# Optimization experiments

Measured on AMD Instinct MI355X. Metric: run time of the kernel, lower is better.

The kernel has to match this reference:

```python
import jax, jax.numpy as jnp
import numpy as np

EMBED = 256
HEADS = 8
HDIM = 32
FF = 1024
EPS = 1e-6
EVERY = 8        # stock_attn_every
LAST_DENSE = 16  # stock_attn_last_dense
B, N, T = 2, 256, 256


def rmsnorm(x, w):
    return x * jax.lax.rsqrt(jnp.mean(x * x, axis=-1, keepdims=True) + EPS) * w


def mha(x, Wq, Wk, Wv, Wo, mask=None):
    # x: (B, S, D); mask: (B, S) bool key-padding mask (True = keep)
    b, s, _ = x.shape
    q = (x @ Wq).reshape(b, s, HEADS, HDIM)
    k = (x @ Wk).reshape(b, s, HEADS, HDIM)
    v = (x @ Wv).reshape(b, s, HEADS, HDIM)
    scores = jnp.einsum('bqhd,bkhd->bhqk', q, k) * (HDIM ** -0.5)
    if mask is not None:
        scores = jnp.where(mask[:, None, None, :], scores, jnp.asarray(-1e9, scores.dtype))
    attn = jax.nn.softmax(scores, axis=-1)
    out = jnp.einsum('bhqk,bkhd->bqhd', attn, v).reshape(b, s, HEADS * HDIM)
    return out @ Wo


def active_t(t):
    # static index set: sparse strided steps + last dense window
    lds = max(0, t - LAST_DENSE)
    idx = sorted(set(list(range(0, lds, max(1, EVERY))) + list(range(lds, t))))
    return jnp.asarray(idx, dtype=jnp.int32)


def setup_inputs() -> dict:
    key = jax.random.key(0)
    ks = jax.random.split(key, 16)
    p = lambda k, shape: (jax.random.normal(k, shape, dtype=jnp.float32) * 0.02)
    inp = {
        'h': jax.random.normal(ks[0], (B, N, T, EMBED), dtype=jnp.float32),
        'stock_mask': jnp.ones((B, N), dtype=jnp.int32),
        'norm_t_w': jnp.ones((EMBED,), dtype=jnp.float32),
        'norm_s_w': jnp.ones((EMBED,), dtype=jnp.float32),
        'norm_ff_w': jnp.ones((EMBED,), dtype=jnp.float32),
        'Wq_t': p(ks[1], (EMBED, HEADS * HDIM)),
        'Wk_t': p(ks[2], (EMBED, HEADS * HDIM)),
        'Wv_t': p(ks[3], (EMBED, HEADS * HDIM)),
        'Wo_t': p(ks[4], (HEADS * HDIM, EMBED)),
        'Wq_s': p(ks[5], (EMBED, HEADS * HDIM)),
        'Wk_s': p(ks[6], (EMBED, HEADS * HDIM)),
        'Wv_s': p(ks[7], (EMBED, HEADS * HDIM)),
        'Wo_s': p(ks[8], (HEADS * HDIM, EMBED)),
        'W1': p(ks[9], (EMBED, FF)),
        'b1': jnp.zeros((FF,), dtype=jnp.float32),
        'W2': p(ks[10], (FF, EMBED)),
        'b2': jnp.zeros((EMBED,), dtype=jnp.float32),
    }
    return inp


def reference(h, stock_mask, norm_t_w, norm_s_w, norm_ff_w,
              Wq_t, Wk_t, Wv_t, Wo_t, Wq_s, Wk_s, Wv_s, Wo_s,
              W1, b1, W2, b2):
    b, n, t, d = h.shape
    # --- time attention (per stock, dense over T) ---
    h_t = rmsnorm(h.reshape(b * n, t, d), norm_t_w)
    h = h + mha(h_t, Wq_t, Wk_t, Wv_t, Wo_t).reshape(b, n, t, d)
    # --- sparse-T gather -> stock attention -> scatter back ---
    active = active_t(t)
    tp = active.shape[0]
    h_s = h[:, :, active, :].transpose(0, 2, 1, 3).reshape(b * tp, n, d)
    m = jnp.broadcast_to(stock_mask.astype(bool)[:, None, :], (b, tp, n)).reshape(b * tp, n)
    h_s = mha(rmsnorm(h_s, norm_s_w), Wq_s, Wk_s, Wv_s, Wo_s, mask=m)
    h = h.at[:, :, active, :].add(h_s.reshape(b, tp, n, d).transpose(0, 2, 1, 3))
    # --- FFN ---
    x = rmsnorm(h, norm_ff_w)
    return h + (jax.nn.gelu(x @ W1 + b1) @ W2 + b2)
```

## Files before the change

### kernel.cpp

```cpp
#include <hip/hip_runtime.h>
#include <hip/hip_bf16.h>

typedef __attribute__((ext_vector_type(8))) short short8;
typedef __attribute__((ext_vector_type(4))) float f32x4;

#define TP 46

__device__ __forceinline__ unsigned short f2bf(float f) {
  unsigned int u = __float_as_uint(f);
  u = (u + 0x7fff + ((u >> 16) & 1)) >> 16;
  return (unsigned short)u;
}
__device__ __forceinline__ unsigned short f2bf_fast(float f) {
  return (unsigned short)((__float_as_uint(f) + 0x8000u) >> 16);
}
__device__ __forceinline__ float bf2f(short u) {
  return __uint_as_float((unsigned)(unsigned short)u << 16);
}
__device__ __forceinline__ float fast_rcp(float x) {
#if __has_builtin(__builtin_amdgcn_rcpf)
  return __builtin_amdgcn_rcpf(x);
#else
  return 1.0f / x;
#endif
}
__device__ __forceinline__ float fast_rsq(float x) {
#if __has_builtin(__builtin_amdgcn_rsqf)
  return __builtin_amdgcn_rsqf(x);
#else
  return rsqrtf(x);
#endif
}

__device__ __forceinline__ int act_t(int j) { return j < 30 ? (j << 3) : (210 + j); }

__device__ __forceinline__ void load_lds16(const unsigned short* g, unsigned short* lds_base) {
#if __has_builtin(__builtin_amdgcn_global_load_lds)
  __builtin_amdgcn_global_load_lds(
      (const __attribute__((address_space(1))) unsigned int*)(unsigned long long)g,
      (__attribute__((address_space(3))) unsigned int*)(unsigned int)(unsigned long long)lds_base,
      16, 0, 0);
#else
  int lane = threadIdx.x & 63;
  *(short8*)(lds_base + lane * 8) = *(const short8*)g;
#endif
}

__global__ __launch_bounds__(256) void convw_kernel(
    const float* __restrict__ wq_t, const float* __restrict__ wk_t,
    const float* __restrict__ wv_t, const float* __restrict__ wo_t,
    const float* __restrict__ wq_s, const float* __restrict__ wk_s,
    const float* __restrict__ wv_s, const float* __restrict__ wo_s,
    const float* __restrict__ w1, const float* __restrict__ w2,
    unsigned short* __restrict__ pool) {
  int idx = blockIdx.x * 256 + threadIdx.x;
  float v;
  if (idx < 524288) {
    int tile = idx >> 12, local = idx & 4095;
    int ks = local >> 9, q = local & 511;
    int l = q >> 3, e = q & 7;
    int lr = l & 15, lg = l >> 4;
    int ct = tile & 15, grp = tile >> 4;
    const float* s = (grp == 0) ? wq_t : (grp == 1) ? wk_t : (grp == 2) ? wv_t :
                     (grp == 3) ? wo_t : (grp == 4) ? wq_s : (grp == 5) ? wk_s :
                     (grp == 6) ? wv_s : wo_s;
    v = s[(size_t)(ks * 32 + lg * 8 + e) * 256 + ct * 16 + lr];
  } else if (idx < 786432) {
    int local = idx - 524288;
    int e = local & 7, t = local >> 3;
    int lane = t & 63, ks = (t >> 6) & 7, ct = (t >> 9) & 1, fc = t >> 10;
    int lr = lane & 15, lg = lane >> 4;
    v = w1[(size_t)(ks * 32 + lg * 8 + e) * 1024 + fc * 32 + ct * 16 + lr];
  } else {
    int local = idx - 786432;
    int e2 = local & 7, t = local >> 3;
    int lane = t & 63, ct2 = (t >> 6) & 15, fc = t >> 10;
    int lr = lane & 15, lg = lane >> 4;
    v = w2[(size_t)(fc * 32 + lg * 8 + e2) * 256 + ct2 * 16 + lr];
  }
  pool[idx] = f2bf(v);
}

template<int GATHER>
__global__ __launch_bounds__(256) void qkv_kernel(
    const float* __restrict__ src, const float* __restrict__ nw,
    const unsigned short* __restrict__ WF,
    unsigned short* __restrict__ qb, unsigned short* __restrict__ kb,
    unsigned short* __restrict__ vb, int row_base) {
  __shared__ __align__(16) unsigned short Wbuf[2][4096];
  int tid = threadIdx.x, wv = tid >> 6, lane = tid & 63, lr = lane & 15, lg = lane >> 4;
  int row0 = blockIdx.x * 128 + wv * 32;
  short8 afrag[2][8];
  #pragma unroll
  for (int rt = 0; rt < 2; ++rt) {
    int lrow = row0 + rt * 16 + lr;
    const float* rp;
    if (GATHER) {
      int gr = row_base + lrow;
      int b = gr / 11776; int rem = gr - b * 11776;
      int j = rem >> 8, n = rem & 255;
      rp = src + (((size_t)((b << 8) + n) << 8) + act_t(j)) * 256;
    } else {
      rp = src + (size_t)lrow * 256;
    }
    float4 x[16];
    #pragma unroll
    for (int ks = 0; ks < 8; ++ks) {
      x[ks * 2]     = *(const float4*)(rp + ks * 32 + lg * 8);
      x[ks * 2 + 1] = *(const float4*)(rp + ks * 32 + lg * 8 + 4);
    }
    float ss = 0.f;
    #pragma unroll
    for (int i = 0; i < 16; ++i)
      ss += x[i].x * x[i].x + x[i].y * x[i].y + x[i].z * x[i].z + x[i].w * x[i].w;
    ss += __shfl_xor(ss, 16, 64);
    ss += __shfl_xor(ss, 32, 64);
    float sc = fast_rsq(ss * 0.00390625f + 1e-6f);
    #pragma unroll
    for (int ks = 0; ks < 8; ++ks) {
      float4 w0 = *(const float4*)(nw + ks * 32 + lg * 8);
      float4 w1_ = *(const float4*)(nw + ks * 32 + lg * 8 + 4);
      short8 af;
      af[0] = (short)f2bf_fast(x[ks * 2].x * sc * w0.x);
      af[1] = (short)f2bf_fast(x[ks * 2].y * sc * w0.y);
      af[2] = (short)f2bf_fast(x[ks * 2].z * sc * w0.z);
      af[3] = (short)f2bf_fast(x[ks * 2].w * sc * w0.w);
      af[4] = (short)f2bf_fast(x[ks * 2 + 1].x * sc * w1_.x);
      af[5] = (short)f2bf_fast(x[ks * 2 + 1].y * sc * w1_.y);
      af[6] = (short)f2bf_fast(x[ks * 2 + 1].z * sc * w1_.z);
      af[7] = (short)f2bf_fast(x[ks * 2 + 1].w * sc * w1_.w);
      afrag[rt][ks] = af;
    }
  }
  #pragma unroll
  for (int i = 0; i < 2; ++i) {
    int s = wv * 2 + i;
    load_lds16(WF + s * 512 + lane * 8, &Wbuf[0][s * 512]);
  }
  f32x4 zero = {0.f, 0.f, 0.f, 0.f};
  for (int t = 0; t < 48; ++t) {
    __syncthreads();
    if (t < 47) {
      #pragma unroll
      for (int i = 0; i < 2; ++i) {
        int s = wv * 2 + i;
        load_lds16(WF + (size_t)(t + 1) * 4096 + s * 512 + lane * 8,
                   &Wbuf[(t + 1) & 1][s * 512]);
      }
    }
    const unsigned short* Ws = &Wbuf[t & 1][0];
    f32x4 a0 = zero, a1 = zero;
    #pragma unroll
    for (int ks = 0; ks < 8; ++ks) {
      short8 bw = *(const short8*)&Ws[ks * 512 + lane * 8];
      a0 = __builtin_amdgcn_mfma_f32_16x16x32_bf16(bw, afrag[0][ks], a0, 0, 0, 0);
      a1 = __builtin_amdgcn_mfma_f32_16x16x32_bf16(bw, afrag[1][ks], a1, 0, 0, 0);
    }
    int m = t >> 4, ct = t & 15;
    unsigned short* dst = (m == 0) ? qb : (m == 1) ? kb : vb;
    ushort4 p0, p1;
    p0.x = f2bf_fast(a0[0]); p0.y = f2bf_fast(a0[1]);
    p0.z = f2bf_fast(a0[2]); p0.w = f2bf_fast(a0[3]);
    p1.x = f2bf_fast(a1[0]); p1.y = f2bf_fast(a1[1]);
    p1.z = f2bf_fast(a1[2]); p1.w = f2bf_fast(a1[3]);
    *(ushort4*)(dst + (size_t)(row0 + lr) * 256 + ct * 16 + lg * 4) = p0;
    *(ushort4*)(dst + (size_t)(row0 + 16 + lr) * 256 + ct * 16 + lg * 4) = p1;
  }
}

template<int MODE>
__global__ __launch_bounds__(256) void gemm256_kernel(
    const unsigned short* __restrict__ X, const unsigned short* __restrict__ WF,
    const float* __restrict__ resid, float* __restrict__ outf, int row_base) {
  __shared__ __align__(16) unsigned short Wbuf[2][4096];
  int tid = threadIdx.x, wv = tid >> 6, lane = tid & 63, lr = lane & 15, lg = lane >> 4;
  int row0 = blockIdx.x * 128 + wv * 32;
  short8 afrag[2][8];
  size_t rb[2];
  #pragma unroll
  for (int rt = 0; rt < 2; ++rt) {
    int row = row0 + rt * 16 + lr;
    #pragma unroll
    for (int ks = 0; ks < 8; ++ks)
      afrag[rt][ks] = *(const short8*)(X + (size_t)row * 256 + ks * 32 + lg * 8);
    if (MODE == 1) {
      rb[rt] = (size_t)row * 256;
    } else {
      int gr = row_base + row;
      int b = gr / 11776; int rem = gr - b * 11776;
      int j = rem >> 8, n = rem & 255;
      rb[rt] = (((size_t)((b << 8) + n) << 8) + act_t(j)) * 256;
    }
  }
  #pragma unroll
  for (int i = 0; i < 2; ++i) {
    int s = wv * 2 + i;
    load_lds16(WF + s * 512 + lane * 8, &Wbuf[0][s * 512]);
  }
  f32x4 zero = {0.f, 0.f, 0.f, 0.f};
  for (int t = 0; t < 16; ++t) {
    __syncthreads();
    if (t < 15) {
      #pragma unroll
      for (int i = 0; i < 2; ++i) {
        int s = wv * 2 + i;
        load_lds16(WF + (size_t)(t + 1) * 4096 + s * 512 + lane * 8,
                   &Wbuf[(t + 1) & 1][s * 512]);
      }
    }
    const unsigned short* Ws = &Wbuf[t & 1][0];
    f32x4 a0 = zero, a1 = zero;
    #pragma unroll
    for (int ks = 0; ks < 8; ++ks) {
      short8 bw = *(const short8*)&Ws[ks * 512 + lane * 8];
      a0 = __builtin_amdgcn_mfma_f32_16x16x32_bf16(bw, afrag[0][ks], a0, 0, 0, 0);
      a1 = __builtin_amdgcn_mfma_f32_16x16x32_bf16(bw, afrag[1][ks], a1, 0, 0, 0);
    }
    int col = t * 16 + lg * 4;
    if (MODE == 1) {
      float4 r0 = *(const float4*)(resid + rb[0] + col);
      float4 r1 = *(const float4*)(resid + rb[1] + col);
      float4 o0, o1;
      o0.x = r0.x + a0[0]; o0.y = r0.y + a0[1]; o0.z = r0.z + a0[2]; o0.w = r0.w + a0[3];
      o1.x = r1.x + a1[0]; o1.y = r1.y + a1[1]; o1.z = r1.z + a1[2]; o1.w = r1.w + a1[3];
      *(float4*)(outf + rb[0] + col) = o0;
      *(float4*)(outf + rb[1] + col) = o1;
    } else {
      float4 c0 = *(const float4*)(outf + rb[0] + col);
      float4 c1 = *(const float4*)(outf + rb[1] + col);
      c0.x += a0[0]; c0.y += a0[1]; c0.z += a0[2]; c0.w += a0[3];
      c1.x += a1[0]; c1.y += a1[1]; c1.z += a1[2]; c1.w += a1[3];
      *(float4*)(outf + rb[0] + col) = c0;
      *(float4*)(outf + rb[1] + col) = c1;
    }
  }
}

__global__ __launch_bounds__(256) void attn_kernel(
    const unsigned short* __restrict__ Q, const unsigned short* __restrict__ K,
    const unsigned short* __restrict__ V, unsigned short* __restrict__ O,
    const int* __restrict__ mask, int seq_base) {
  __shared__ unsigned short Ksh[256][40];
  __shared__ unsigned short Vtsh[32][264];
  __shared__ unsigned short Psh[4][16][264];
  int head = blockIdx.x, seq = blockIdx.y;
  int hc = head * 32;
  size_t sb = (size_t)seq * 65536;
  int tid = threadIdx.x;
  {
    int r = tid;
    #pragma unroll
    for (int c = 0; c < 4; ++c) {
      *(short8*)&Ksh[r][c * 8] = *(const short8*)(K + sb + (size_t)r * 256 + hc + c * 8);
      short8 vv = *(const short8*)(V + sb + (size_t)r * 256 + hc + c * 8);
      #pragma unroll
      for (int e = 0; e < 8; ++e) Vtsh[c * 8 + e][r] = (unsigned short)vv[e];
    }
  }
  __syncthreads();
  int wv = tid >> 6, lane = tid & 63, lr = lane & 15, lg = lane >> 4;
  const float scale = 0.17677669529663687f;
  int mb = 0;
  if (mask) mb = (seq_base + seq) / TP;
  f32x4 zero = {0.f, 0.f, 0.f, 0.f};
  for (int rt = 0; rt < 4; ++rt) {
    int row0 = wv * 64 + rt * 16;
    short8 aq = *(const short8*)(Q + sb + (size_t)(row0 + lr) * 256 + hc + lg * 8);
    f32x4 s[16];
    #pragma unroll
    for (int ct = 0; ct < 16; ++ct) {
      short8 kb = *(const short8*)&Ksh[ct * 16 + lr][lg * 8];
      s[ct] = __builtin_amdgcn_mfma_f32_16x16x32_bf16(kb, aq, zero, 0, 0, 0);
    }
    #pragma unroll
    for (int ct = 0; ct < 16; ++ct) {
      if (mask) {
        const int4 m4 = *(const int4*)(mask + mb * 256 + ct * 16 + lg * 4);
        s[ct][0] = m4.x ? s[ct][0] * scale : -1e9f;
        s[ct][1] = m4.y ? s[ct][1] * scale : -1e9f;
        s[ct][2] = m4.z ? s[ct][2] * scale : -1e9f;
        s[ct][3] = m4.w ? s[ct][3] * scale : -1e9f;
      } else {
        #pragma unroll
        for (int r = 0; r < 4; ++r) s[ct][r] *= scale;
      }
    }
    float mx = -3e38f;
    #pragma unroll
    for (int ct = 0; ct < 16; ++ct)
      #pragma unroll
      for (int r = 0; r < 4; ++r) mx = fmaxf(mx, s[ct][r]);
    mx = fmaxf(mx, __shfl_xor(mx, 16, 64));
    mx = fmaxf(mx, __shfl_xor(mx, 32, 64));
    float sum = 0.f;
    #pragma unroll
    for (int ct = 0; ct < 16; ++ct)
      #pragma unroll
      for (int r = 0; r < 4; ++r) {
        float p = __expf(s[ct][r] - mx);
        s[ct][r] = p; sum += p;
      }
    sum += __shfl_xor(sum, 16, 64);
    sum += __shfl_xor(sum, 32, 64);
    float inv = fast_rcp(sum);
    #pragma unroll
    for (int ct = 0; ct < 16; ++ct) {
      ushort4 pk;
      pk.x = f2bf_fast(s[ct][0] * inv); pk.y = f2bf_fast(s[ct][1] * inv);
      pk.z = f2bf_fast(s[ct][2] * inv); pk.w = f2bf_fast(s[ct][3] * inv);
      *(ushort4*)&Psh[wv][lr][ct * 16 + lg * 4] = pk;
    }
    f32x4 o[2] = {zero, zero};
    #pragma unroll
    for (int ks = 0; ks < 8; ++ks) {
      short8 pa = *(const short8*)&Psh[wv][lr][ks * 32 + lg * 8];
      #pragma unroll
      for (int c2 = 0; c2 < 2; ++c2) {
        short8 vbf = *(const short8*)&Vtsh[c2 * 16 + lr][ks * 32 + lg * 8];
        o[c2] = __builtin_amdgcn_mfma_f32_16x16x32_bf16(vbf, pa, o[c2], 0, 0, 0);
      }
    }
    #pragma unroll
    for (int c2 = 0; c2 < 2; ++c2) {
      ushort4 ok;
      ok.x = f2bf_fast(o[c2][0]); ok.y = f2bf_fast(o[c2][1]);
      ok.z = f2bf_fast(o[c2][2]); ok.w = f2bf_fast(o[c2][3]);
      *(ushort4*)(O + sb + (size_t)(row0 + lr) * 256 + hc + c2 * 16 + lg * 4) = ok;
    }
  }
}

__global__ __launch_bounds__(256, 4) void ffn_kernel(
    float* __restrict__ hio, const float* __restrict__ nw,
    const unsigned short* __restrict__ W1F, const unsigned short* __restrict__ W2F,
    const float* __restrict__ b1, const float* __restrict__ b2) {
  __shared__ __align__(16) unsigned short Wbuf[16384];
  __shared__ __align__(16) unsigned short Psh[4][16][36];
  int tid = threadIdx.x;
  int wv = tid >> 6, lane = tid & 63, lr = lane & 15, lg = lane >> 4;
  int wrow = blockIdx.x * 64 + wv * 16;
  const float* rp = hio + (size_t)(wrow + lr) * 256;
  short8 xfrag[8];
  float ss = 0.f;
  #pragma unroll
  for (int ks = 0; ks < 8; ++ks) {
    float4 a = *(const float4*)(rp + ks * 32 + lg * 8);
    float4 b = *(const float4*)(rp + ks * 32 + lg * 8 + 4);
    ss += a.x * a.x + a.y * a.y + a.z * a.z + a.w * a.w;
    ss += b.x * b.x + b.y * b.y + b.z * b.z + b.w * b.w;
    short8 xf;
    xf[0] = (short)f2bf_fast(a.x); xf[1] = (short)f2bf_fast(a.y);
    xf[2] = (short)f2bf_fast(a.z); xf[3] = (short)f2bf_fast(a.w);
    xf[4] = (short)f2bf_fast(b.x); xf[5] = (short)f2bf_fast(b.y);
    xf[6] = (short)f2bf_fast(b.z); xf[7] = (short)f2bf_fast(b.w);
    xfrag[ks] = xf;
  }
  ss += __shfl_xor(ss, 16, 64);
  ss += __shfl_xor(ss, 32, 64);
  float sc = fast_rsq(ss * 0.00390625f + 1e-6f);
  #pragma unroll
  for (int ks = 0; ks < 8; ++ks) {
    float4 wa = *(const float4*)(nw + ks * 32 + lg * 8);
    float4 wb = *(const float4*)(nw + ks * 32 + lg * 8 + 4);
    short8 xf = xfrag[ks], af;
    af[0] = (short)f2bf_fast(bf2f(xf[0]) * sc * wa.x);
    af[1] = (short)f2bf_fast(bf2f(xf[1]) * sc * wa.y);
    af[2] = (short)f2bf_fast(bf2f(xf[2]) * sc * wa.z);
    af[3] = (short)f2bf_fast(bf2f(xf[3]) * sc * wa.w);
    af[4] = (short)f2bf_fast(bf2f(xf[4]) * sc * wb.x);
    af[5] = (short)f2bf_fast(bf2f(xf[5]) * sc * wb.y);
    af[6] = (short)f2bf_fast(bf2f(xf[6]) * sc * wb.z);
    af[7] = (short)f2bf_fast(bf2f(xf[7]) * sc * wb.w);
    xfrag[ks] = af;
  }
  f32x4 zero = {0.f, 0.f, 0.f, 0.f};
  f32x4 oacc[16];
  #pragma unroll
  for (int ct = 0; ct < 16; ++ct) oacc[ct] = zero;
  for (int fc = 0; fc < 32; ++fc) {
    __syncthreads();
    #pragma unroll
    for (int i = 0; i < 8; ++i) {
      int s = wv * 8 + i;
      const unsigned short* srcp = (s < 16) ? (W1F + (size_t)fc * 8192 + s * 512)
                                            : (W2F + (size_t)fc * 8192 + (s - 16) * 512);
      load_lds16(srcp + lane * 8, &Wbuf[s * 512]);
    }
    __syncthreads();
    const unsigned short* W1s = &Wbuf[0];
    const unsigned short* W2s = &Wbuf[8192];
    f32x4 hacc[2];
    hacc[0] = zero; hacc[1] = zero;
    #pragma unroll
    for (int ks = 0; ks < 8; ++ks) {
      #pragma unroll
      for (int ct = 0; ct < 2; ++ct) {
        short8 w1f = *(const short8*)&W1s[(ct * 8 + ks) * 512 + lane * 8];
        hacc[ct] = __builtin_amdgcn_mfma_f32_16x16x32_bf16(w1f, xfrag[ks], hacc[ct], 0, 0, 0);
      }
    }
    #pragma unroll
    for (int ct = 0; ct < 2; ++ct) {
      float4 bb = *(const float4*)(b1 + fc * 32 + ct * 16 + lg * 4);
      ushort4 pk;
      float hv = hacc[ct][0] + bb.x;
      pk.x = f2bf_fast(hv * fast_rcp(1.0f + __expf(-1.5957691216057308f * fmaf(0.044715f * hv, hv * hv, hv))));
      hv = hacc[ct][1] + bb.y;
      pk.y = f2bf_fast(hv * fast_rcp(1.0f + __expf(-1.5957691216057308f * fmaf(0.044715f * hv, hv * hv, hv))));
      hv = hacc[ct][2] + bb.z;
      pk.z = f2bf_fast(hv * fast_rcp(1.0f + __expf(-1.5957691216057308f * fmaf(0.044715f * hv, hv * hv, hv))));
      hv = hacc[ct][3] + bb.w;
      pk.w = f2bf_fast(hv * fast_rcp(1.0f + __expf(-1.5957691216057308f * fmaf(0.044715f * hv, hv * hv, hv))));
      *(ushort4*)&Psh[wv][lr][ct * 16 + lg * 4] = pk;
    }
    short8 pa = *(const short8*)&Psh[wv][lr][lg * 8];
    #pragma unroll
    for (int ct2 = 0; ct2 < 16; ++ct2) {
      short8 bw2 = *(const short8*)&W2s[ct2 * 512 + lane * 8];
      oacc[ct2] = __builtin_amdgcn_mfma_f32_16x16x32_bf16(bw2, pa, oacc[ct2], 0, 0, 0);
    }
  }
  size_t rbase = (size_t)(wrow + lr) * 256;
  #pragma unroll
  for (int ct2 = 0; ct2 < 16; ++ct2) {
    int col = ct2 * 16 + lg * 4;
    float4 bb2 = *(const float4*)(b2 + col);
    float4 cur = *(const float4*)(hio + rbase + col);
    cur.x += oacc[ct2][0] + bb2.x;
    cur.y += oacc[ct2][1] + bb2.y;
    cur.z += oacc[ct2][2] + bb2.z;
    cur.w += oacc[ct2][3] + bb2.w;
    *(float4*)(hio + rbase + col) = cur;
  }
}

extern "C" void kernel_launch(void* const* d_in, const int* in_sizes, int n_in,
                              void* d_out, int out_size, void* d_ws, size_t ws_size,
                              hipStream_t stream) {
  (void)in_sizes; (void)n_in; (void)out_size;
  const float* h   = (const float*)d_in[0];
  const int* smask = (const int*)d_in[1];
  const float* ntw = (const float*)d_in[2];
  const float* nsw = (const float*)d_in[3];
  const float* nfw = (const float*)d_in[4];
  const float* wq_t = (const float*)d_in[5];
  const float* wk_t = (const float*)d_in[6];
  const float* wv_t = (const float*)d_in[7];
  const float* wo_t = (const float*)d_in[8];
  const float* wq_s = (const float*)d_in[9];
  const float* wk_s = (const float*)d_in[10];
  const float* wv_s = (const float*)d_in[11];
  const float* wo_s = (const float*)d_in[12];
  const float* w1  = (const float*)d_in[13];
  const float* b1  = (const float*)d_in[14];
  const float* w2  = (const float*)d_in[15];
  const float* b2  = (const float*)d_in[16];
  float* out = (float*)d_out;
  unsigned short* pool = (unsigned short*)d_ws;

  unsigned short* WQKVtF = pool;
  unsigned short* WOtF   = pool + 196608;
  unsigned short* WQKVsF = pool + 262144;
  unsigned short* WOsF   = pool + 458752;
  unsigned short* W1F    = pool + 524288;
  unsigned short* W2F    = pool + 786432;

  size_t wbytes = 1048576ull * 2;
  size_t avail = (ws_size > wbytes) ? (ws_size - wbytes) : 0;
  long long scl = (long long)(avail / 524288ull);
  int SC = scl < 1 ? 1 : (scl > 512 ? 512 : (int)scl);
  unsigned short* xnorm = pool + 1048576;
  unsigned short* qb = xnorm + (size_t)SC * 65536;
  unsigned short* kb = qb + (size_t)SC * 65536;
  unsigned short* vb = kb + (size_t)SC * 65536;

  convw_kernel<<<4096, 256, 0, stream>>>(wq_t, wk_t, wv_t, wo_t, wq_s, wk_s, wv_s,
                                         wo_s, w1, w2, pool);

  for (int s0 = 0; s0 < 512; s0 += SC) {
    int ns = (512 - s0 < SC) ? (512 - s0) : SC;
    int rows = ns * 256;
    qkv_kernel<0><<<rows / 128, 256, 0, stream>>>(h + (size_t)s0 * 65536, ntw, WQKVtF,
                                                  qb, kb, vb, 0);
    attn_kernel<<<dim3(8, ns), 256, 0, stream>>>(qb, kb, vb, xnorm, nullptr, 0);
    gemm256_kernel<1><<<rows / 128, 256, 0, stream>>>(xnorm, WOtF,
        h + (size_t)s0 * 65536, out + (size_t)s0 * 65536, 0);
  }

  int SC2 = SC < 92 ? SC : 92;
  for (int s0 = 0; s0 < 92; s0 += SC2) {
    int ns = (92 - s0 < SC2) ? (92 - s0) : SC2;
    int rows = ns * 256;
    qkv_kernel<1><<<rows / 128, 256, 0, stream>>>(out, nsw, WQKVsF, qb, kb, vb, s0 * 256);
    attn_kernel<<<dim3(8, ns), 256, 0, stream>>>(qb, kb, vb, xnorm, smask, s0);
    gemm256_kernel<2><<<rows / 128, 256, 0, stream>>>(xnorm, WOsF, nullptr, out, s0 * 256);
  }

  ffn_kernel<<<2048, 256, 0, stream>>>(out, nfw, W1F, W2F, b1, b2);
}
```

Before: 755.7 us.

## Double-buffer FFN weight tiles with manual vmcnt waits and template attention mask

The FFN kernel now double-buffers its W1/W2 LDS tiles, prefetching the next chunk while computing the current one. It uses raw s_barrier plus s_waitcnt vmcnt instead of full __syncthreads, and caches b1 in shared memory. The qkv kernel gets the same finer-grained waits, the attention kernel takes the mask as a template parameter and uses a coalesced K/V load pattern, and the FFN launch is split into two halves. The double buffer doubles FFN LDS use, which may lower occupancy, and the hand-written waitcnt counts must match the number of outstanding loads or results will be wrong.

Measured after the change: 835.8 us. 10.6% more time.

```diff
diff --git a/kernel.cpp b/kernel.cpp
--- a/kernel.cpp
+++ b/kernel.cpp
@@ -5,6 +5,11 @@
 typedef __attribute__((ext_vector_type(4))) float f32x4;
 
 #define TP 46
+
+#define SBAR() asm volatile("s_barrier" ::: "memory")
+#define VMCNT2() asm volatile("s_waitcnt vmcnt(2)" ::: "memory")
+#define VMCNT8() asm volatile("s_waitcnt vmcnt(8)" ::: "memory")
+#define VMCNT0() asm volatile("s_waitcnt vmcnt(0)" ::: "memory")
 
 __device__ __forceinline__ unsigned short f2bf(float f) {
   unsigned int u = __float_as_uint(f);
@@ -139,7 +144,7 @@
   }
   f32x4 zero = {0.f, 0.f, 0.f, 0.f};
   for (int t = 0; t < 48; ++t) {
-    __syncthreads();
+    SBAR();
     if (t < 47) {
       #pragma unroll
       for (int i = 0; i < 2; ++i) {
@@ -147,7 +152,11 @@
         load_lds16(WF + (size_t)(t + 1) * 4096 + s * 512 + lane * 8,
                    &Wbuf[(t + 1) & 1][s * 512]);
       }
-    }
+      VMCNT2();
+    } else {
+      VMCNT0();
+    }
+    SBAR();
     const unsigned short* Ws = &Wbuf[t & 1][0];
     f32x4 a0 = zero, a1 = zero;
     #pragma unroll
@@ -208,6 +217,7 @@
                    &Wbuf[(t + 1) & 1][s * 512]);
       }
     }
+    __syncthreads();
     const unsigned short* Ws = &Wbuf[t & 1][0];
     f32x4 a0 = zero, a1 = zero;
     #pragma unroll
@@ -236,6 +246,7 @@
   }
 }
 
+template<int MASKED>
 __global__ __launch_bounds__(256) void attn_kernel(
     const unsigned short* __restrict__ Q, const unsigned short* __restrict__ K,
     const unsigned short* __restrict__ V, unsigned short* __restrict__ O,
@@ -248,9 +259,10 @@
   size_t sb = (size_t)seq * 65536;
   int tid = threadIdx.x;
   {
-    int r = tid;
-    #pragma unroll
-    for (int c = 0; c < 4; ++c) {
+    int c = tid & 3, rbase = tid >> 2;
+    #pragma unroll
+    for (int i = 0; i < 4; ++i) {
+      int r = rbase + i * 64;
       *(short8*)&Ksh[r][c * 8] = *(const short8*)(K + sb + (size_t)r * 256 + hc + c * 8);
       short8 vv = *(const short8*)(V + sb + (size_t)r * 256 + hc + c * 8);
       #pragma unroll
@@ -261,7 +273,7 @@
   int wv = tid >> 6, lane = tid & 63, lr = lane & 15, lg = lane >> 4;
   const float scale = 0.17677669529663687f;
   int mb = 0;
-  if (mask) mb = (seq_base + seq) / TP;
+  if (MASKED) mb = (seq_base + seq) / TP;
   f32x4 zero = {0.f, 0.f, 0.f, 0.f};
   for (int rt = 0; rt < 4; ++rt) {
     int row0 = wv * 64 + rt * 16;
@@ -274,7 +286,7 @@
     }
     #pragma unroll
     for (int ct = 0; ct < 16; ++ct) {
-      if (mask) {
+      if (MASKED) {
         const int4 m4 = *(const int4*)(mask + mb * 256 + ct * 16 + lg * 4);
         s[ct][0] = m4.x ? s[ct][0] * scale : -1e9f;
         s[ct][1] = m4.y ? s[ct][1] * scale : -1e9f;
@@ -334,8 +346,9 @@
     float* __restrict__ hio, const float* __restrict__ nw,
     const unsigned short* __restrict__ W1F, const unsigned short* __restrict__ W2F,
     const float* __restrict__ b1, const float* __restrict__ b2) {
-  __shared__ __align__(16) unsigned short Wbuf[16384];
+  __shared__ __align__(16) unsigned short Wbuf[2][16384];
   __shared__ __align__(16) unsigned short Psh[4][16][36];
+  __shared__ __align__(16) float b1sh[1024];
   int tid = threadIdx.x;
   int wv = tid >> 6, lane = tid & 63, lr = lane & 15, lg = lane >> 4;
   int wrow = blockIdx.x * 64 + wv * 16;
@@ -373,22 +386,37 @@
     af[7] = (short)f2bf_fast(bf2f(xf[7]) * sc * wb.w);
     xfrag[ks] = af;
   }
+  *(float4*)&b1sh[tid * 4] = *(const float4*)(b1 + tid * 4);
+  __syncthreads();
+  #pragma unroll
+  for (int i = 0; i < 8; ++i) {
+    int s = wv * 8 + i;
+    const unsigned short* srcp = (s < 16) ? (W1F + (size_t)s * 512)
+                                          : (W2F + (size_t)(s - 16) * 512);
+    load_lds16(srcp + lane * 8, &Wbuf[0][s * 512]);
+  }
   f32x4 zero = {0.f, 0.f, 0.f, 0.f};
   f32x4 oacc[16];
   #pragma unroll
   for (int ct = 0; ct < 16; ++ct) oacc[ct] = zero;
   for (int fc = 0; fc < 32; ++fc) {
-    __syncthreads();
-    #pragma unroll
-    for (int i = 0; i < 8; ++i) {
-      int s = wv * 8 + i;
-      const unsigned short* srcp = (s < 16) ? (W1F + (size_t)fc * 8192 + s * 512)
-                                            : (W2F + (size_t)fc * 8192 + (s - 16) * 512);
-      load_lds16(srcp + lane * 8, &Wbuf[s * 512]);
-    }
-    __syncthreads();
-    const unsigned short* W1s = &Wbuf[0];
-    const unsigned short* W2s = &Wbuf[8192];
+    SBAR();
+    if (fc < 31) {
+      size_t go = (size_t)(fc + 1) * 8192;
+      #pragma unroll
+      for (int i = 0; i < 8; ++i) {
+        int s = wv * 8 + i;
+        const unsigned short* srcp = (s < 16) ? (W1F + go + (size_t)s * 512)
+                                              : (W2F + go + (size_t)(s - 16) * 512);
+        load_lds16(srcp + lane * 8, &Wbuf[(fc + 1) & 1][s * 512]);
+      }
+      VMCNT8();
+    } else {
+      VMCNT0();
+    }
+    SBAR();
+    const unsigned short* W1s = &Wbuf[fc & 1][0];
+    const unsigned short* W2s = &Wbuf[fc & 1][8192];
     f32x4 hacc[2];
     hacc[0] = zero; hacc[1] = zero;
     #pragma unroll
@@ -401,7 +429,7 @@
     }
     #pragma unroll
     for (int ct = 0; ct < 2; ++ct) {
-      float4 bb = *(const float4*)(b1 + fc * 32 + ct * 16 + lg * 4);
+      float4 bb = *(const float4*)&b1sh[fc * 32 + ct * 16 + lg * 4];
       ushort4 pk;
       float hv = hacc[ct][0] + bb.x;
       pk.x = f2bf_fast(hv * fast_rcp(1.0f + __expf(-1.5957691216057308f * fmaf(0.044715f * hv, hv * hv, hv))));
@@ -482,7 +510,7 @@
     int rows = ns * 256;
     qkv_kernel<0><<<rows / 128, 256, 0, stream>>>(h + (size_t)s0 * 65536, ntw, WQKVtF,
                                                   qb, kb, vb, 0);
-    attn_kernel<<<dim3(8, ns), 256, 0, stream>>>(qb, kb, vb, xnorm, nullptr, 0);
+    attn_kernel<0><<<dim3(8, ns), 256, 0, stream>>>(qb, kb, vb, xnorm, nullptr, 0);
     gemm256_kernel<1><<<rows / 128, 256, 0, stream>>>(xnorm, WOtF,
         h + (size_t)s0 * 65536, out + (size_t)s0 * 65536, 0);
   }
@@ -492,9 +520,10 @@
     int ns = (92 - s0 < SC2) ? (92 - s0) : SC2;
     int rows = ns * 256;
     qkv_kernel<1><<<rows / 128, 256, 0, stream>>>(out, nsw, WQKVsF, qb, kb, vb, s0 * 256);
-    attn_kernel<<<dim3(8, ns), 256, 0, stream>>>(qb, kb, vb, xnorm, smask, s0);
+    attn_kernel<1><<<dim3(8, ns), 256, 0, stream>>>(qb, kb, vb, xnorm, smask, s0);
     gemm256_kernel<2><<<rows / 128, 256, 0, stream>>>(xnorm, WOsF, nullptr, out, s0 * 256);
   }
 
-  ffn_kernel<<<2048, 256, 0, stream>>>(out, nfw, W1F, W2F, b1, b2);
-}
+  ffn_kernel<<<1024, 256, 0, stream>>>(out, nfw, W1F, W2F, b1, b2);
+  ffn_kernel<<<1024, 256, 0, stream>>>(out + 16777216ull, nfw, W1F, W2F, b1, b2);
+}
```
